# Optimization experiments

Measured on AMD Instinct MI355X. Metric: run time of the kernel, lower is better.

The kernel has to match this reference:

```python
import jax, jax.numpy as jnp
import numpy as np

LS = (0, 1, 2, 3)                 # spherical-harmonic degrees of edge_attrs
DIMS = [2 * l + 1 for l in LS]    # [1,3,5,7], total 16
OFFS = np.cumsum([0] + DIMS)      # slice offsets into the SH axis
C = 128                           # node feature channels (128x0e)
C_DOWN = 64                       # node_feats_down_irreps = 64x0e
N_BESSEL = 8                      # edge_feats_irreps = 8x0e
AVG_NUM_NEIGHBORS = 10.0


def setup_inputs() -> dict:
    key = jax.random.key(0)
    ks = jax.random.split(key, 14)
    N, E = 10000, 100000
    node_attrs = jax.random.normal(ks[0], (N, 10), jnp.float32)
    node_feats = jax.random.normal(ks[1], (N, C), jnp.float32)
    edge_attrs = jax.random.normal(ks[2], (E, sum(DIMS)), jnp.float32)
    edge_feats = jax.random.normal(ks[3], (E, N_BESSEL), jnp.float32)
    edge_index = jax.random.randint(ks[4], (2, E), 0, N, dtype=jnp.int32)
    inv_c = 1.0 / np.sqrt(C)
    W_up = jax.random.normal(ks[5], (C, C), jnp.float32) * inv_c
    W_down = jax.random.normal(ks[6], (C, C_DOWN), jnp.float32) * inv_c
    W_skip = jax.random.normal(ks[7], (C, C), jnp.float32) * inv_c
    # FullyConnectedNet dims: [8 + 2*64] + 3*[256] + [weight_numel = 4*C]
    dims = [N_BESSEL + 2 * C_DOWN, 256, 256, 256, len(LS) * C]
    W_fc0 = jax.random.normal(ks[8], (dims[0], dims[1]), jnp.float32)
    W_fc1 = jax.random.normal(ks[9], (dims[1], dims[2]), jnp.float32)
    W_fc2 = jax.random.normal(ks[10], (dims[2], dims[3]), jnp.float32)
    W_fc3 = jax.random.normal(ks[11], (dims[3], dims[4]), jnp.float32)
    # final Linear(irreps_mid -> target): independent channel mixing per l
    W_out = jax.random.normal(ks[12], (len(LS), C, C), jnp.float32) * inv_c
    return dict(node_attrs=node_attrs, node_feats=node_feats, edge_attrs=edge_attrs,
                edge_feats=edge_feats, edge_index=edge_index,
                W_up=W_up, W_down=W_down, W_skip=W_skip,
                W_fc0=W_fc0, W_fc1=W_fc1, W_fc2=W_fc2, W_fc3=W_fc3, W_out=W_out)


def reference(node_attrs, node_feats, edge_attrs, edge_feats, edge_index,
              W_up, W_down, W_skip, W_fc0, W_fc1, W_fc2, W_fc3, W_out):
    sender = edge_index[0]
    receiver = edge_index[1]
    N = node_feats.shape[0]

    # skip connection (e3nn Linear on 0e channels)
    sc = node_feats @ W_skip                                   # [N, C]
    x_up = node_feats @ W_up                                   # [N, C]
    x_down = node_feats @ W_down                               # [N, 64]

    # radial weight network on augmented edge features
    aug = jnp.concatenate([edge_feats, x_down[sender], x_down[receiver]], axis=-1)  # [E, 136]
    h = aug
    for W in (W_fc0, W_fc1, W_fc2):
        h = jax.nn.silu(h @ (W / jnp.sqrt(jnp.asarray(W.shape[0], h.dtype))))
    tp_w = h @ (W_fc3 / jnp.sqrt(jnp.asarray(W_fc3.shape[0], h.dtype)))  # [E, 4*C]
    tp_w = tp_w.reshape(-1, len(LS), C)                        # [E, 4, C]

    # per-edge 'uvu' tensor product: 128x0e (gathered sender) x SH(lmax=3)
    xs = x_up[sender]                                          # [E, C]
    parts = []
    for i, l in enumerate(LS):
        Y = edge_attrs[:, OFFS[i]:OFFS[i + 1]]                 # [E, 2l+1]
        cg = 1.0 / np.sqrt(2 * l + 1)                          # w3j(0,l,l)
        part = (tp_w[:, i, :] * xs)[:, :, None] * (Y * cg)[:, None, :]  # [E, C, 2l+1]
        parts.append(part.reshape(part.shape[0], C * (2 * l + 1)))
    mji = jnp.concatenate(parts, axis=-1)                      # [E, C*16]

    # scatter-sum to receivers
    message = jax.ops.segment_sum(mji, receiver, num_segments=N)  # [N, C*16]

    # per-l channel-mixing linear, then / avg_num_neighbors, then reshape_irreps
    outs = []
    off = 0
    for i, l in enumerate(LS):
        d = 2 * l + 1
        blk = message[:, off:off + C * d].reshape(N, C, d)
        outs.append(jnp.einsum('ncd,ck->nkd', blk, W_out[i]))
        off += C * d
    out = jnp.concatenate(outs, axis=-1) / AVG_NUM_NEIGHBORS   # [N, C, 16]
    return out, sc
```

## Files before the change

kernel.cpp:

```cpp
#include <hip/hip_runtime.h>
#include <math.h>

using bf16x8 = __attribute__((ext_vector_type(8))) short;
using f32x4  = __attribute__((ext_vector_type(4))) float;

__device__ __forceinline__ float silu_f(float x) {
    float e = __expf(-x);
    float d = 1.f + e;
    return x * __builtin_amdgcn_rcpf(d);
}

__device__ __forceinline__ unsigned short f2bf(float x) {
    union { float f; unsigned u; } v; v.f = x;
    unsigned u = v.u;
    return (unsigned short)((u + 0x7FFFu + ((u >> 16) & 1u)) >> 16);
}
__device__ __forceinline__ unsigned f2bf2(float lo, float hi) {
    return (unsigned)f2bf(lo) | ((unsigned)f2bf(hi) << 16);
}
__device__ __forceinline__ float bf2f(unsigned short h) {
    union { unsigned u; float f; } v; v.u = ((unsigned)h) << 16;
    return v.f;
}

__global__ __launch_bounds__(256) void k_node_gemm(
    const float* __restrict__ A,
    const float* __restrict__ Wskip, const float* __restrict__ Wup, const float* __restrict__ Wdown,
    float* __restrict__ sc, float* __restrict__ xup, float* __restrict__ xdown, int N)
{
    __shared__ float As[64][129];
    const int t = threadIdx.x;
    const int n0 = blockIdx.x * 64;
    for (int i = t; i < 64 * 32; i += 256) {
        int r = i >> 5, c4 = i & 31;
        int n = n0 + r;
        float4 v = make_float4(0.f, 0.f, 0.f, 0.f);
        if (n < N) v = ((const float4*)(A + (size_t)n * 128))[c4];
        As[r][c4 * 4 + 0] = v.x; As[r][c4 * 4 + 1] = v.y;
        As[r][c4 * 4 + 2] = v.z; As[r][c4 * 4 + 3] = v.w;
    }
    __syncthreads();
    const int tc = t & 15, tr = t >> 4;
    const int col0 = blockIdx.y * 64 + tc * 4;
    const float* W; float* dst; int ldw, wc, ldd;
    if (col0 < 128)      { W = Wskip; ldw = 128; wc = col0;       dst = sc;    ldd = 128; }
    else if (col0 < 256) { W = Wup;   ldw = 128; wc = col0 - 128; dst = xup;   ldd = 128; }
    else                 { W = Wdown; ldw = 64;  wc = col0 - 256; dst = xdown; ldd = 64;  }
    float acc[4][4] = {};
    for (int k = 0; k < 128; k++) {
        float4 wv = *(const float4*)(W + (size_t)k * ldw + wc);
        float wvv[4] = {wv.x, wv.y, wv.z, wv.w};
        float av[4];
        #pragma unroll
        for (int ii = 0; ii < 4; ii++) av[ii] = As[tr * 4 + ii][k];
        #pragma unroll
        for (int ii = 0; ii < 4; ii++)
            #pragma unroll
            for (int jj = 0; jj < 4; jj++)
                acc[ii][jj] = fmaf(av[ii], wvv[jj], acc[ii][jj]);
    }
    #pragma unroll
    for (int ii = 0; ii < 4; ii++) {
        int n = n0 + tr * 4 + ii;
        if (n < N)
            *(float4*)(dst + (size_t)n * ldd + wc) =
                make_float4(acc[ii][0], acc[ii][1], acc[ii][2], acc[ii][3]);
    }
}

__global__ __launch_bounds__(256) void k_prep_w(
    const float* __restrict__ W, unsigned short* __restrict__ Wt,
    int Kin, int Kpad, int Nout, float scale)
{
    int i = blockIdx.x * 256 + threadIdx.x;
    if (i >= Nout * Kpad) return;
    int n = i / Kpad, k = i - n * Kpad;
    float v = (k < Kin) ? W[(size_t)k * Nout + n] * scale : 0.f;
    Wt[i] = f2bf(v);
}

#define MEB 128

__global__ __launch_bounds__(512, 2) void k_mlp_mfma(
    const float* __restrict__ ef, const int* __restrict__ eidx,
    const float* __restrict__ xdown,
    const unsigned short* __restrict__ Wt0, const unsigned short* __restrict__ Wt1,
    const unsigned short* __restrict__ Wt2, const unsigned short* __restrict__ Wt3,
    unsigned short* __restrict__ tp_w, int E, int eLo, int eHi)
{
    __shared__ unsigned short bufA[MEB][264];
    __shared__ unsigned short bufB[MEB][264];
    __shared__ int sE[MEB], rE[MEB];
    const int t = threadIdx.x;
    const int w = t >> 6, lane = t & 63;
    const int rA = lane & 15;
    const int kb = (lane >> 4) * 8;
    const int r0 = (lane >> 4) * 4;
    const int e0 = eLo + blockIdx.x * MEB;

    bf16x8 bw[16];
    f32x4 acc[8][2];

#define LOADW(WT, KPADW, NKS)                                                     \
    _Pragma("unroll")                                                             \
    for (int ks = 0; ks < NKS; ks++)                                              \
        _Pragma("unroll")                                                         \
        for (int nt = 0; nt < 2; nt++)                                            \
            bw[ks * 2 + nt] = *(const bf16x8*)&(WT)[(size_t)(w * 32 + nt * 16 + rA) * (KPADW) + ks * 32 + kb];

#define LMFMA(IN, NKS)                                                            \
    _Pragma("unroll")                                                             \
    for (int mt = 0; mt < 8; mt++)                                                \
        _Pragma("unroll")                                                         \
        for (int nt = 0; nt < 2; nt++)                                            \
            acc[mt][nt] = (f32x4){0.f, 0.f, 0.f, 0.f};                            \
    _Pragma("unroll")                                                             \
    for (int ks = 0; ks < NKS; ks++) {                                            \
        const int kk = ks * 32 + kb;                                              \
        bf16x8 afr[8];                                                            \
        _Pragma("unroll")                                                         \
        for (int mt = 0; mt < 8; mt++)                                            \
            afr[mt] = *(const bf16x8*)&IN[mt * 16 + rA][kk];                      \
        _Pragma("unroll")                                                         \
        for (int mt = 0; mt < 8; mt++)                                            \
            _Pragma("unroll")                                                     \
            for (int nt = 0; nt < 2; nt++)                                        \
                acc[mt][nt] = __builtin_amdgcn_mfma_f32_16x16x32_bf16(afr[mt], bw[ks * 2 + nt], acc[mt][nt], 0, 0, 0); \
    }

#define EPILOG(OUT, DOSILU)                                                       \
    _Pragma("unroll")                                                             \
    for (int mt = 0; mt < 8; mt++)                                                \
        _Pragma("unroll")                                                         \
        for (int nt = 0; nt < 2; nt++) {                                          \
            const int col = w * 32 + nt * 16 + rA;                                \
            _Pragma("unroll")                                                     \
            for (int r = 0; r < 4; r++) {                                         \
                float x = acc[mt][nt][r];                                         \
                if (DOSILU) x = silu_f(x);                                        \
                OUT[mt * 16 + r0 + r][col] = f2bf(x);                             \
            }                                                                     \
        }

    if (t < MEB) {
        int e = e0 + t; if (e >= E) e = E - 1;
        sE[t] = eidx[e]; rE[t] = eidx[E + e];
    }
    __syncthreads();
    for (int i = t; i < MEB * 24; i += 512) {
        int r = i / 24, c = 136 + i % 24;
        bufA[r][c] = 0;
    }
    for (int i = t; i < MEB * 34; i += 512) {
        int e = i / 34, j = i - e * 34;
        float4 v;
        if (j < 2) { int ee = e0 + e; if (ee >= E) ee = E - 1; v = ((const float4*)(ef + (size_t)ee * 8))[j]; }
        else if (j < 18) v = ((const float4*)(xdown + (size_t)sE[e] * 64))[j - 2];
        else             v = ((const float4*)(xdown + (size_t)rE[e] * 64))[j - 18];
        unsigned lo = f2bf2(v.x, v.y), hi = f2bf2(v.z, v.w);
        *(uint2*)&bufA[e][j * 4] = make_uint2(lo, hi);
    }
    __syncthreads();

    LOADW(Wt0, 160, 5)
    LMFMA(bufA, 5)
    EPILOG(bufB, true)
    __syncthreads();

    LOADW(Wt1, 256, 8)
    LMFMA(bufB, 8)
    EPILOG(bufA, true)
    __syncthreads();

    LOADW(Wt2, 256, 8)
    LMFMA(bufA, 8)
    EPILOG(bufB, true)
    __syncthreads();

    LOADW(Wt3, 256, 8)
    LMFMA(bufB, 8)
    EPILOG(bufA, false)
    __syncthreads();
    for (int i = t; i < MEB * 64; i += 512) {
        int r = i >> 6, c4 = i & 63;
        int ee = e0 + r;
        if (ee < eHi) {
            ushort4 hv = *(ushort4*)&bufA[r][c4 * 4];
            *(ushort4*)&tp_w[(size_t)(ee - eLo) * 512 + c4 * 4] = hv;
        }
    }
    __syncthreads();

    LOADW(Wt3 + (size_t)256 * 256, 256, 8)
    LMFMA(bufB, 8)
    EPILOG(bufA, false)
    __syncthreads();
    for (int i = t; i < MEB * 64; i += 512) {
        int r = i >> 6, c4 = i & 63;
        int ee = e0 + r;
        if (ee < eHi) {
            ushort4 hv = *(ushort4*)&bufA[r][c4 * 4];
            *(ushort4*)&tp_w[(size_t)(ee - eLo) * 512 + 256 + c4 * 4] = hv;
        }
    }
#undef LOADW
#undef LMFMA
#undef EPILOG
}

__global__ __launch_bounds__(256, 2) void k_zx(
    unsigned short* __restrict__ tpw, const int* __restrict__ eidx,
    const float* __restrict__ xup, const unsigned short* __restrict__ WoT,
    int E, int eLo, int eHi)
{
    __shared__ __align__(16) unsigned short As[128 * 128];
    __shared__ __align__(16) unsigned short Bs[128 * 128];
    const int t = threadIdx.x;
    const int m0 = blockIdx.x * 128;
    const int l  = blockIdx.y;
    const int nE = eHi - eLo;

    #pragma unroll
    for (int i = 0; i < 8; i++) {
        int idx = i * 256 + t;
        int r = idx >> 4, cc = idx & 15;
        int el = m0 + r;
        int ecl = el < nE ? el : nE - 1;
        int s = eidx[eLo + ecl];
        uint4 tv = *(const uint4*)(tpw + (size_t)ecl * 512 + l * 128 + (cc << 3));
        float4 x0 = *(const float4*)(xup + (size_t)s * 128 + (cc << 3));
        float4 x1 = *(const float4*)(xup + (size_t)s * 128 + (cc << 3) + 4);
        const unsigned short* hp = (const unsigned short*)&tv;
        uint4 ov;
        unsigned* op = (unsigned*)&ov;
        op[0] = f2bf2(bf2f(hp[0]) * x0.x, bf2f(hp[1]) * x0.y);
        op[1] = f2bf2(bf2f(hp[2]) * x0.z, bf2f(hp[3]) * x0.w);
        op[2] = f2bf2(bf2f(hp[4]) * x1.x, bf2f(hp[5]) * x1.y);
        op[3] = f2bf2(bf2f(hp[6]) * x1.z, bf2f(hp[7]) * x1.w);
        *(uint4*)(&As[r * 128 + ((cc ^ (r & 7)) << 3)]) = ov;
    }
    #pragma unroll
    for (int i = 0; i < 8; i++) {
        int idx = i * 256 + t;
        int r = idx >> 4, cc = idx & 15;
        uint4 bv = *(const uint4*)(WoT + ((size_t)l * 128 + r) * 128 + (cc << 3));
        *(uint4*)(&Bs[r * 128 + ((cc ^ (r & 7)) << 3)]) = bv;
    }
    __syncthreads();

    const int lane = t & 63, rA = lane & 15, q = lane >> 4;
    const int wm = (t >> 6) & 1, wn = (t >> 6) >> 1;
    f32x4 acc[4][4];
    #pragma unroll
    for (int mt = 0; mt < 4; mt++)
        #pragma unroll
        for (int nt = 0; nt < 4; nt++)
            acc[mt][nt] = (f32x4){0.f, 0.f, 0.f, 0.f};

    #pragma unroll
    for (int ks = 0; ks < 4; ks++) {
        const int cc = ks * 4 + q;
        bf16x8 af[4], bfr[4];
        #pragma unroll
        for (int mt = 0; mt < 4; mt++) {
            int row = wm * 64 + mt * 16 + rA;
            af[mt] = *(const bf16x8*)&As[row * 128 + ((cc ^ (row & 7)) << 3)];
        }
        #pragma unroll
        for (int nt = 0; nt < 4; nt++) {
            int row = wn * 64 + nt * 16 + rA;
            bfr[nt] = *(const bf16x8*)&Bs[row * 128 + ((cc ^ (row & 7)) << 3)];
        }
        #pragma unroll
        for (int mt = 0; mt < 4; mt++)
            #pragma unroll
            for (int nt = 0; nt < 4; nt++)
                acc[mt][nt] = __builtin_amdgcn_mfma_f32_16x16x32_bf16(af[mt], bfr[nt], acc[mt][nt], 0, 0, 0);
    }
    __syncthreads();

    #pragma unroll
    for (int mt = 0; mt < 4; mt++) {
        #pragma unroll
        for (int r = 0; r < 4; r++) {
            int row = m0 + wm * 64 + mt * 16 + q * 4 + r;
            if (row >= nE) continue;
            #pragma unroll
            for (int nt = 0; nt < 4; nt++) {
                int col = wn * 64 + nt * 16 + rA;
                tpw[(size_t)row * 512 + l * 128 + col] = f2bf(acc[mt][nt][r]);
            }
        }
    }
}

__global__ __launch_bounds__(256) void k_hist(const int* __restrict__ recv, int* __restrict__ deg, int E)
{
    int e = blockIdx.x * 256 + threadIdx.x;
    if (e < E) atomicAdd(&deg[recv[e]], 1);
}

__global__ __launch_bounds__(1024) void k_scan(const int* __restrict__ deg, int* __restrict__ rowptr, int N)
{
    __shared__ int sdata[1024];
    __shared__ int carry;
    const int t = threadIdx.x;
    if (t == 0) carry = 0;
    __syncthreads();
    for (int base = 0; base < N; base += 1024) {
        int i = base + t;
        int v = (i < N) ? deg[i] : 0;
        sdata[t] = v;
        __syncthreads();
        for (int off = 1; off < 1024; off <<= 1) {
            int x = (t >= off) ? sdata[t - off] : 0;
            __syncthreads();
            sdata[t] += x;
            __syncthreads();
        }
        if (i < N) rowptr[i] = carry + sdata[t] - v;
        __syncthreads();
        if (t == 0) carry += sdata[1023];
        __syncthreads();
    }
    if (t == 0) rowptr[N] = carry;
}

__global__ __launch_bounds__(256) void k_scatter(const int* __restrict__ recv,
    const int* __restrict__ rowptr, int* __restrict__ fill, int* __restrict__ perm, int E)
{
    int e = blockIdx.x * 256 + threadIdx.x;
    if (e < E) {
        int r = recv[e];
        int pos = rowptr[r] + atomicAdd(&fill[r], 1);
        perm[pos] = e;
    }
}

__global__ __launch_bounds__(256) void k_sortlists(int* __restrict__ perm, const int* __restrict__ rowptr, int N)
{
    int n = blockIdx.x * 256 + threadIdx.x;
    if (n >= N) return;
    int lo = rowptr[n], hi = rowptr[n + 1];
    for (int i = lo + 1; i < hi; i++) {
        int key = perm[i];
        int j = i - 1;
        while (j >= lo && perm[j] > key) { perm[j + 1] = perm[j]; j--; }
        perm[j + 1] = key;
    }
}

__global__ __launch_bounds__(256) void k_gather(
    const unsigned short* __restrict__ z, const float* __restrict__ ea,
    const int* __restrict__ perm, const int* __restrict__ rowptr,
    float* __restrict__ outb, int E, int eLo, int eHi, int storeMode)
{
    const int n = blockIdx.x;
    const int lo = rowptr[n], hi = rowptr[n + 1];
    const int t = threadIdx.x;
    const int c = t & 127, half = t >> 7;
    const int nE = eHi - eLo;
    constexpr float CG1 = 0.57735026919f, CG2 = 0.44721359550f, CG3 = 0.37796447301f;
    float acc[8] = {};
    __shared__ int eG[64];
    __shared__ int eL[64];
    __shared__ float yL[64][17];
    for (int base = lo; base < hi; base += 64) {
        int cnt = min(64, hi - base);
        for (int i = t; i < cnt; i += 256) {
            int e = perm[base + i];
            eG[i] = e;
            int el = e - eLo;
            eL[i] = (el >= 0 && el < nE) ? el : 0;
        }
        __syncthreads();
        for (int i = t; i < cnt * 16; i += 256) {
            int el = i >> 4, m = i & 15;
            int e = eG[el];
            float v = ea[(size_t)e * 16 + m];
            yL[el][m] = (e >= eLo && e < eHi) ? v : 0.f;
        }
        __syncthreads();
        int j = 0;
        for (; j + 4 <= cnt; j += 4) {
            const unsigned short* zp[4];
            #pragma unroll
            for (int k = 0; k < 4; k++) zp[k] = z + (size_t)eL[j + k] * 512;
            if (half == 0) {
                float z0[4], z1[4], z2[4];
                #pragma unroll
                for (int k = 0; k < 4; k++) {
                    z0[k] = bf2f(zp[k][c]);
                    z1[k] = bf2f(zp[k][128 + c]);
                    z2[k] = bf2f(zp[k][256 + c]);
                }
                #pragma unroll
                for (int k = 0; k < 4; k++) {
                    const float* y = yL[j + k];
                    float u1 = z1[k] * CG1, u2 = z2[k] * CG2;
                    acc[0] = fmaf(z0[k], y[0], acc[0]);
                    #pragma unroll
                    for (int m = 0; m < 3; m++) acc[1 + m] = fmaf(u1, y[1 + m], acc[1 + m]);
                    #pragma unroll
                    for (int m = 0; m < 4; m++) acc[4 + m] = fmaf(u2, y[4 + m], acc[4 + m]);
                }
            } else {
                float z2[4], z3[4];
                #pragma unroll
                for (int k = 0; k < 4; k++) {
                    z2[k] = bf2f(zp[k][256 + c]);
                    z3[k] = bf2f(zp[k][384 + c]);
                }
                #pragma unroll
                for (int k = 0; k < 4; k++) {
                    const float* y = yL[j + k];
                    float u2 = z2[k] * CG2, u3 = z3[k] * CG3;
                    acc[0] = fmaf(u2, y[8], acc[0]);
                    #pragma unroll
                    for (int m = 0; m < 7; m++) acc[1 + m] = fmaf(u3, y[9 + m], acc[1 + m]);
                }
            }
        }
        for (; j < cnt; j++) {
            const unsigned short* zz = z + (size_t)eL[j] * 512;
            const float* y = yL[j];
            if (half == 0) {
                float z0 = bf2f(zz[c]);
                float z1 = bf2f(zz[128 + c]) * CG1;
                float z2 = bf2f(zz[256 + c]) * CG2;
                acc[0] = fmaf(z0, y[0], acc[0]);
                #pragma unroll
                for (int m = 0; m < 3; m++) acc[1 + m] = fmaf(z1, y[1 + m], acc[1 + m]);
                #pragma unroll
                for (int m = 0; m < 4; m++) acc[4 + m] = fmaf(z2, y[4 + m], acc[4 + m]);
            } else {
                float z2 = bf2f(zz[256 + c]) * CG2;
                float z3 = bf2f(zz[384 + c]) * CG3;
                acc[0] = fmaf(z2, y[8], acc[0]);
                #pragma unroll
                for (int m = 0; m < 7; m++) acc[1 + m] = fmaf(z3, y[9 + m], acc[1 + m]);
            }
        }
        __syncthreads();
    }
    float* orow = outb + (size_t)n * 2048 + (size_t)c * 16 + half * 8;
    if (storeMode) {
        *(float4*)orow       = make_float4(acc[0], acc[1], acc[2], acc[3]);
        *(float4*)(orow + 4) = make_float4(acc[4], acc[5], acc[6], acc[7]);
    } else {
        float4 a = *(float4*)orow, b = *(float4*)(orow + 4);
        a.x += acc[0]; a.y += acc[1]; a.z += acc[2]; a.w += acc[3];
        b.x += acc[4]; b.y += acc[5]; b.z += acc[6]; b.w += acc[7];
        *(float4*)orow = a; *(float4*)(orow + 4) = b;
    }
}

extern "C" void kernel_launch(void* const* d_in, const int* in_sizes, int n_in,
                              void* d_out, int out_size, void* d_ws, size_t ws_size,
                              hipStream_t stream)
{
    const float* node_feats = (const float*)d_in[1];
    const float* edge_attrs = (const float*)d_in[2];
    const float* edge_feats = (const float*)d_in[3];
    const int*   edge_index = (const int*)d_in[4];
    const float* W_up   = (const float*)d_in[5];
    const float* W_down = (const float*)d_in[6];
    const float* W_skip = (const float*)d_in[7];
    const float* W_fc0  = (const float*)d_in[8];
    const float* W_fc1  = (const float*)d_in[9];
    const float* W_fc2  = (const float*)d_in[10];
    const float* W_fc3  = (const float*)d_in[11];
    const float* W_out  = (const float*)d_in[12];
    const int N = in_sizes[1] / 128;
    const int E = in_sizes[3] / 8;

    float* out = (float*)d_out;
    float* sc  = out + (size_t)N * 2048;

    float* xup   = (float*)d_ws;
    float* xdown = xup + (size_t)N * 128;
    int* deg    = (int*)(xdown + (size_t)N * 64);
    int* fill   = deg + N;
    int* rowptr = fill + N;
    int* perm   = rowptr + N + 1;
    size_t used = (size_t)((char*)(perm + E) - (char*)d_ws);
    used = (used + 255) & ~(size_t)255;
    unsigned short* Wt0 = (unsigned short*)((char*)d_ws + used);
    unsigned short* Wt1 = Wt0 + 256 * 160;
    unsigned short* Wt2 = Wt1 + 256 * 256;
    unsigned short* Wt3 = Wt2 + 256 * 256;
    unsigned short* WoT = Wt3 + 512 * 256;
    used = (size_t)((char*)(WoT + 4 * 128 * 128) - (char*)d_ws);
    used = (used + 255) & ~(size_t)255;
    unsigned short* tpw = (unsigned short*)((char*)d_ws + used);
    size_t avail = (ws_size > used) ? ws_size - used : 0;
    long long Ec_l = (long long)(avail / (512 * sizeof(unsigned short)));
    int Ec = (int)(Ec_l > E ? E : Ec_l);
    if (Ec < 8) Ec = 8;
    const int nchunks = (E + Ec - 1) / Ec;

    hipMemsetAsync(deg, 0, (size_t)2 * N * sizeof(int), stream);
    if (nchunks > 1)
        hipMemsetAsync(out, 0, (size_t)N * 2048 * sizeof(float), stream);

    dim3 g1((N + 63) / 64, 5);
    k_node_gemm<<<g1, 256, 0, stream>>>(node_feats, W_skip, W_up, W_down, sc, xup, xdown, N);

    constexpr float S0 = 0.085749292571254f;
    k_prep_w<<<(256 * 160 + 255) / 256, 256, 0, stream>>>(W_fc0, Wt0, 136, 160, 256, S0);
    k_prep_w<<<(256 * 256 + 255) / 256, 256, 0, stream>>>(W_fc1, Wt1, 256, 256, 256, 0.0625f);
    k_prep_w<<<(256 * 256 + 255) / 256, 256, 0, stream>>>(W_fc2, Wt2, 256, 256, 256, 0.0625f);
    k_prep_w<<<(512 * 256 + 255) / 256, 256, 0, stream>>>(W_fc3, Wt3, 256, 256, 512, 0.0625f);
    for (int l = 0; l < 4; l++)
        k_prep_w<<<(128 * 128 + 255) / 256, 256, 0, stream>>>(W_out + (size_t)l * 16384,
                                                              WoT + (size_t)l * 16384,
                                                              128, 128, 128, 0.1f);

    const int* recv = edge_index + E;
    k_hist<<<(E + 255) / 256, 256, 0, stream>>>(recv, deg, E);
    k_scan<<<1, 1024, 0, stream>>>(deg, rowptr, N);
    k_scatter<<<(E + 255) / 256, 256, 0, stream>>>(recv, rowptr, fill, perm, E);
    k_sortlists<<<(N + 255) / 256, 256, 0, stream>>>(perm, rowptr, N);

    for (int ch = 0; ch < nchunks; ch++) {
        int eLo = ch * Ec;
        int eHi = eLo + Ec; if (eHi > E) eHi = E;
        int nE = eHi - eLo;

        k_mlp_mfma<<<(nE + MEB - 1) / MEB, 512, 0, stream>>>(edge_feats, edge_index, xdown,
                                                             Wt0, Wt1, Wt2, Wt3,
                                                             tpw, E, eLo, eHi);
        k_zx<<<dim3((nE + 127) / 128, 4), 256, 0, stream>>>(tpw, edge_index, xup, WoT,
                                                            E, eLo, eHi);
        k_gather<<<N, 256, 0, stream>>>(tpw, edge_attrs, perm, rowptr,
                                        out, E, eLo, eHi, nchunks == 1 ? 1 : 0);
    }
}
```

Before: 354.3 us.

## Fuse sender-feature multiply into MLP epilogue and shrink gather blocks to one wave

Moves the elementwise multiply of tp_w by the gathered sender x_up row out of k_zx and into the k_mlp_mfma store epilogue, so k_zx only copies the premultiplied bf16 tile into LDS and no longer reads edge_index or x_up. The gather kernel is restructured to 64 threads per node, with each thread handling two channels and all four l-blocks instead of splitting l across half-blocks. This drops redundant index and x_up loads in k_zx and gives each gather thread more work and fewer idle lanes. In exchange, the MLP epilogue does extra x_up reads and conversions, and the smaller gather blocks may hide memory latency less well.

```diff
diff --git a/kernel.cpp b/kernel.cpp
--- a/kernel.cpp
+++ b/kernel.cpp
@@ -83,10 +83,10 @@
 
 __global__ __launch_bounds__(512, 2) void k_mlp_mfma(
     const float* __restrict__ ef, const int* __restrict__ eidx,
-    const float* __restrict__ xdown,
+    const float* __restrict__ xdown, const float* __restrict__ xup,
     const unsigned short* __restrict__ Wt0, const unsigned short* __restrict__ Wt1,
     const unsigned short* __restrict__ Wt2, const unsigned short* __restrict__ Wt3,
-    unsigned short* __restrict__ tp_w, int E, int eLo, int eHi)
+    unsigned short* __restrict__ ubuf, int E, int eLo, int eHi)
 {
     __shared__ unsigned short bufA[MEB][264];
     __shared__ unsigned short bufB[MEB][264];
@@ -97,6 +97,7 @@
     const int kb = (lane >> 4) * 8;
     const int r0 = (lane >> 4) * 4;
     const int e0 = eLo + blockIdx.x * MEB;
+    const float4* __restrict__ xupv = (const float4*)xup;
 
     bf16x8 bw[16];
     f32x4 acc[8][2];
@@ -185,8 +186,11 @@
         int r = i >> 6, c4 = i & 63;
         int ee = e0 + r;
         if (ee < eHi) {
+            float4 xv = xupv[(size_t)sE[r] * 32 + (c4 & 31)];
             ushort4 hv = *(ushort4*)&bufA[r][c4 * 4];
-            *(ushort4*)&tp_w[(size_t)(ee - eLo) * 512 + c4 * 4] = hv;
+            unsigned lo = f2bf2(bf2f(hv.x) * xv.x, bf2f(hv.y) * xv.y);
+            unsigned hi = f2bf2(bf2f(hv.z) * xv.z, bf2f(hv.w) * xv.w);
+            *(uint2*)&ubuf[(size_t)(ee - eLo) * 512 + c4 * 4] = make_uint2(lo, hi);
         }
     }
     __syncthreads();
@@ -199,8 +203,11 @@
         int r = i >> 6, c4 = i & 63;
         int ee = e0 + r;
         if (ee < eHi) {
+            float4 xv = xupv[(size_t)sE[r] * 32 + (c4 & 31)];
             ushort4 hv = *(ushort4*)&bufA[r][c4 * 4];
-            *(ushort4*)&tp_w[(size_t)(ee - eLo) * 512 + 256 + c4 * 4] = hv;
+            unsigned lo = f2bf2(bf2f(hv.x) * xv.x, bf2f(hv.y) * xv.y);
+            unsigned hi = f2bf2(bf2f(hv.z) * xv.z, bf2f(hv.w) * xv.w);
+            *(uint2*)&ubuf[(size_t)(ee - eLo) * 512 + 256 + c4 * 4] = make_uint2(lo, hi);
         }
     }
 #undef LOADW
@@ -209,8 +216,7 @@
 }
 
 __global__ __launch_bounds__(256, 2) void k_zx(
-    unsigned short* __restrict__ tpw, const int* __restrict__ eidx,
-    const float* __restrict__ xup, const unsigned short* __restrict__ WoT,
+    unsigned short* __restrict__ ubuf, const unsigned short* __restrict__ WoT,
     int E, int eLo, int eHi)
 {
     __shared__ __align__(16) unsigned short As[128 * 128];
@@ -226,18 +232,8 @@
         int r = idx >> 4, cc = idx & 15;
         int el = m0 + r;
         int ecl = el < nE ? el : nE - 1;
-        int s = eidx[eLo + ecl];
-        uint4 tv = *(const uint4*)(tpw + (size_t)ecl * 512 + l * 128 + (cc << 3));
-        float4 x0 = *(const float4*)(xup + (size_t)s * 128 + (cc << 3));
-        float4 x1 = *(const float4*)(xup + (size_t)s * 128 + (cc << 3) + 4);
-        const unsigned short* hp = (const unsigned short*)&tv;
-        uint4 ov;
-        unsigned* op = (unsigned*)&ov;
-        op[0] = f2bf2(bf2f(hp[0]) * x0.x, bf2f(hp[1]) * x0.y);
-        op[1] = f2bf2(bf2f(hp[2]) * x0.z, bf2f(hp[3]) * x0.w);
-        op[2] = f2bf2(bf2f(hp[4]) * x1.x, bf2f(hp[5]) * x1.y);
-        op[3] = f2bf2(bf2f(hp[6]) * x1.z, bf2f(hp[7]) * x1.w);
-        *(uint4*)(&As[r * 128 + ((cc ^ (r & 7)) << 3)]) = ov;
+        uint4 tv = *(const uint4*)(ubuf + (size_t)ecl * 512 + l * 128 + (cc << 3));
+        *(uint4*)(&As[r * 128 + ((cc ^ (r & 7)) << 3)]) = tv;
     }
     #pragma unroll
     for (int i = 0; i < 8; i++) {
@@ -288,7 +284,7 @@
             #pragma unroll
             for (int nt = 0; nt < 4; nt++) {
                 int col = wn * 64 + nt * 16 + rA;
-                tpw[(size_t)row * 512 + l * 128 + col] = f2bf(acc[mt][nt][r]);
+                ubuf[(size_t)row * 512 + l * 128 + col] = f2bf(acc[mt][nt][r]);
             }
         }
     }
@@ -350,7 +346,7 @@
     }
 }
 
-__global__ __launch_bounds__(256) void k_gather(
+__global__ __launch_bounds__(64) void k_gather(
     const unsigned short* __restrict__ z, const float* __restrict__ ea,
     const int* __restrict__ perm, const int* __restrict__ rowptr,
     float* __restrict__ outb, int E, int eLo, int eHi, int storeMode)
@@ -358,100 +354,106 @@
     const int n = blockIdx.x;
     const int lo = rowptr[n], hi = rowptr[n + 1];
     const int t = threadIdx.x;
-    const int c = t & 127, half = t >> 7;
     const int nE = eHi - eLo;
     constexpr float CG1 = 0.57735026919f, CG2 = 0.44721359550f, CG3 = 0.37796447301f;
-    float acc[8] = {};
+    float acc[2][2][8] = {};
     __shared__ int eG[64];
     __shared__ int eL[64];
     __shared__ float yL[64][17];
+
     for (int base = lo; base < hi; base += 64) {
         int cnt = min(64, hi - base);
-        for (int i = t; i < cnt; i += 256) {
+        __syncthreads();
+        for (int i = t; i < cnt; i += 64) {
             int e = perm[base + i];
             eG[i] = e;
             int el = e - eLo;
             eL[i] = (el >= 0 && el < nE) ? el : 0;
         }
         __syncthreads();
-        for (int i = t; i < cnt * 16; i += 256) {
+        for (int i = t; i < cnt * 16; i += 64) {
             int el = i >> 4, m = i & 15;
             int e = eG[el];
             float v = ea[(size_t)e * 16 + m];
             yL[el][m] = (e >= eLo && e < eHi) ? v : 0.f;
         }
         __syncthreads();
+
         int j = 0;
         for (; j + 4 <= cnt; j += 4) {
-            const unsigned short* zp[4];
+            float zv[4][8];
             #pragma unroll
-            for (int k = 0; k < 4; k++) zp[k] = z + (size_t)eL[j + k] * 512;
-            if (half == 0) {
-                float z0[4], z1[4], z2[4];
+            for (int k = 0; k < 4; k++) {
+                const unsigned short* zz = z + (size_t)eL[j + k] * 512;
+                zv[k][0] = bf2f(zz[t]);
+                zv[k][1] = bf2f(zz[128 + t]);
+                zv[k][2] = bf2f(zz[256 + t]);
+                zv[k][3] = bf2f(zz[384 + t]);
+                zv[k][4] = bf2f(zz[64 + t]);
+                zv[k][5] = bf2f(zz[192 + t]);
+                zv[k][6] = bf2f(zz[320 + t]);
+                zv[k][7] = bf2f(zz[448 + t]);
+            }
+            #pragma unroll
+            for (int k = 0; k < 4; k++) {
+                const float* y = yL[j + k];
                 #pragma unroll
-                for (int k = 0; k < 4; k++) {
-                    z0[k] = bf2f(zp[k][c]);
-                    z1[k] = bf2f(zp[k][128 + c]);
-                    z2[k] = bf2f(zp[k][256 + c]);
-                }
-                #pragma unroll
-                for (int k = 0; k < 4; k++) {
-                    const float* y = yL[j + k];
-                    float u1 = z1[k] * CG1, u2 = z2[k] * CG2;
-                    acc[0] = fmaf(z0[k], y[0], acc[0]);
+                for (int ci = 0; ci < 2; ci++) {
+                    float z0 = zv[k][ci * 4 + 0];
+                    float z1 = zv[k][ci * 4 + 1] * CG1;
+                    float z2 = zv[k][ci * 4 + 2] * CG2;
+                    float z3 = zv[k][ci * 4 + 3] * CG3;
+                    acc[ci][0][0] = fmaf(z0, y[0], acc[ci][0][0]);
                     #pragma unroll
-                    for (int m = 0; m < 3; m++) acc[1 + m] = fmaf(u1, y[1 + m], acc[1 + m]);
+                    for (int m = 0; m < 3; m++) acc[ci][0][1 + m] = fmaf(z1, y[1 + m], acc[ci][0][1 + m]);
                     #pragma unroll
-                    for (int m = 0; m < 4; m++) acc[4 + m] = fmaf(u2, y[4 + m], acc[4 + m]);
-                }
-            } else {
-                float z2[4], z3[4];
-                #pragma unroll
-                for (int k = 0; k < 4; k++) {
-                    z2[k] = bf2f(zp[k][256 + c]);
-                    z3[k] = bf2f(zp[k][384 + c]);
-                }
-                #pragma unroll
-                for (int k = 0; k < 4; k++) {
-                    const float* y = yL[j + k];
-                    float u2 = z2[k] * CG2, u3 = z3[k] * CG3;
-                    acc[0] = fmaf(u2, y[8], acc[0]);
+                    for (int m = 0; m < 4; m++) acc[ci][0][4 + m] = fmaf(z2, y[4 + m], acc[ci][0][4 + m]);
+                    acc[ci][1][0] = fmaf(z2, y[8], acc[ci][1][0]);
                     #pragma unroll
-                    for (int m = 0; m < 7; m++) acc[1 + m] = fmaf(u3, y[9 + m], acc[1 + m]);
+                    for (int m = 0; m < 7; m++) acc[ci][1][1 + m] = fmaf(z3, y[9 + m], acc[ci][1][1 + m]);
                 }
             }
         }
         for (; j < cnt; j++) {
             const unsigned short* zz = z + (size_t)eL[j] * 512;
             const float* y = yL[j];
-            if (half == 0) {
+            #pragma unroll
+            for (int ci = 0; ci < 2; ci++) {
+                int c = t + ci * 64;
                 float z0 = bf2f(zz[c]);
                 float z1 = bf2f(zz[128 + c]) * CG1;
                 float z2 = bf2f(zz[256 + c]) * CG2;
-                acc[0] = fmaf(z0, y[0], acc[0]);
+                float z3 = bf2f(zz[384 + c]) * CG3;
+                acc[ci][0][0] = fmaf(z0, y[0], acc[ci][0][0]);
                 #pragma unroll
-                for (int m = 0; m < 3; m++) acc[1 + m] = fmaf(z1, y[1 + m], acc[1 + m]);
+                for (int m = 0; m < 3; m++) acc[ci][0][1 + m] = fmaf(z1, y[1 + m], acc[ci][0][1 + m]);
                 #pragma unroll
-                for (int m = 0; m < 4; m++) acc[4 + m] = fmaf(z2, y[4 + m], acc[4 + m]);
-            } else {
-                float z2 = bf2f(zz[256 + c]) * CG2;
-                float z3 = bf2f(zz[384 + c]) * CG3;
-                acc[0] = fmaf(z2, y[8], acc[0]);
+                for (int m = 0; m < 4; m++) acc[ci][0][4 + m] = fmaf(z2, y[4 + m], acc[ci][0][4 + m]);
+                acc[ci][1][0] = fmaf(z2, y[8], acc[ci][1][0]);
                 #pragma unroll
-                for (int m = 0; m < 7; m++) acc[1 + m] = fmaf(z3, y[9 + m], acc[1 + m]);
+                for (int m = 0; m < 7; m++) acc[ci][1][1 + m] = fmaf(z3, y[9 + m], acc[ci][1][1 + m]);
             }
         }
-        __syncthreads();
-    }
-    float* orow = outb + (size_t)n * 2048 + (size_t)c * 16 + half * 8;
-    if (storeMode) {
-        *(float4*)orow       = make_float4(acc[0], acc[1], acc[2], acc[3]);
-        *(float4*)(orow + 4) = make_float4(acc[4], acc[5], acc[6], acc[7]);
-    } else {
-        float4 a = *(float4*)orow, b = *(float4*)(orow + 4);
-        a.x += acc[0]; a.y += acc[1]; a.z += acc[2]; a.w += acc[3];
-        b.x += acc[4]; b.y += acc[5]; b.z += acc[6]; b.w += acc[7];
-        *(float4*)orow = a; *(float4*)(orow + 4) = b;
+    }
+
+    #pragma unroll
+    for (int ci = 0; ci < 2; ci++) {
+        float* orow = outb + (size_t)n * 2048 + (size_t)(t + ci * 64) * 16;
+        if (storeMode) {
+            *(float4*)(orow)      = make_float4(acc[ci][0][0], acc[ci][0][1], acc[ci][0][2], acc[ci][0][3]);
+            *(float4*)(orow + 4)  = make_float4(acc[ci][0][4], acc[ci][0][5], acc[ci][0][6], acc[ci][0][7]);
+            *(float4*)(orow + 8)  = make_float4(acc[ci][1][0], acc[ci][1][1], acc[ci][1][2], acc[ci][1][3]);
+            *(float4*)(orow + 12) = make_float4(acc[ci][1][4], acc[ci][1][5], acc[ci][1][6], acc[ci][1][7]);
+        } else {
+            float4 a = *(float4*)(orow), b = *(float4*)(orow + 4);
+            float4 cc = *(float4*)(orow + 8), d = *(float4*)(orow + 12);
+            a.x += acc[ci][0][0]; a.y += acc[ci][0][1]; a.z += acc[ci][0][2]; a.w += acc[ci][0][3];
+            b.x += acc[ci][0][4]; b.y += acc[ci][0][5]; b.z += acc[ci][0][6]; b.w += acc[ci][0][7];
+            cc.x += acc[ci][1][0]; cc.y += acc[ci][1][1]; cc.z += acc[ci][1][2]; cc.w += acc[ci][1][3];
+            d.x += acc[ci][1][4]; d.y += acc[ci][1][5]; d.z += acc[ci][1][6]; d.w += acc[ci][1][7];
+            *(float4*)(orow) = a; *(float4*)(orow + 4) = b;
+            *(float4*)(orow + 8) = cc; *(float4*)(orow + 12) = d;
+        }
     }
 }
 
@@ -492,7 +494,7 @@
     unsigned short* WoT = Wt3 + 512 * 256;
     used = (size_t)((char*)(WoT + 4 * 128 * 128) - (char*)d_ws);
     used = (used + 255) & ~(size_t)255;
-    unsigned short* tpw = (unsigned short*)((char*)d_ws + used);
+    unsigned short* ubuf = (unsigned short*)((char*)d_ws + used);
     size_t avail = (ws_size > used) ? ws_size - used : 0;
     long long Ec_l = (long long)(avail / (512 * sizeof(unsigned short)));
     int Ec = (int)(Ec_l > E ? E : Ec_l);
@@ -527,12 +529,11 @@
         int eHi = eLo + Ec; if (eHi > E) eHi = E;
         int nE = eHi - eLo;
 
-        k_mlp_mfma<<<(nE + MEB - 1) / MEB, 512, 0, stream>>>(edge_feats, edge_index, xdown,
+        k_mlp_mfma<<<(nE + MEB - 1) / MEB, 512, 0, stream>>>(edge_feats, edge_index, xdown, xup,
                                                              Wt0, Wt1, Wt2, Wt3,
-                                                             tpw, E, eLo, eHi);
-        k_zx<<<dim3((nE + 127) / 128, 4), 256, 0, stream>>>(tpw, edge_index, xup, WoT,
-                                                            E, eLo, eHi);
-        k_gather<<<N, 256, 0, stream>>>(tpw, edge_attrs, perm, rowptr,
-                                        out, E, eLo, eHi, nchunks == 1 ? 1 : 0);
-    }
-}
+                                                             ubuf, E, eLo, eHi);
+        k_zx<<<dim3((nE + 127) / 128, 4), 256, 0, stream>>>(ubuf, WoT, E, eLo, eHi);
+        k_gather<<<N, 64, 0, stream>>>(ubuf, edge_attrs, perm, rowptr,
+                                       out, E, eLo, eHi, nchunks == 1 ? 1 : 0);
+    }
+}
```

Measured after the change: 369.3 us. +4.2%, slower.
